# Performance work log

Hardware: AMD Instinct MI355X
Metric: run time of the kernel (lower is better)

The kernel has to match this reference:

```python
import jax, jax.numpy as jnp
import numpy as np

D = 768
H = 12
HD = D // H
NQ = 100
KV = 257
SEQ = NQ + KV
BS = 32


def layer_norm(x, g, b):
    # torch LayerNorm computed in fp32 then cast back (LayerNorm subclass)
    xf = x.astype(jnp.float32)
    m = xf.mean(-1, keepdims=True)
    v = ((xf - m) ** 2).mean(-1, keepdims=True)
    return ((xf - m) / jnp.sqrt(v + 1e-5) * g + b).astype(x.dtype)


def setup_inputs() -> dict:
    key = jax.random.key(0)
    ks = jax.random.split(key, 8)
    s = 0.02
    return {
        "y": jax.random.normal(ks[0], (SEQ, BS, D), jnp.float32),
        "attn_mask": jax.random.bernoulli(ks[1], 0.3, (BS, NQ, KV)),
        "in_proj_w": jax.random.normal(ks[2], (3 * D, D), jnp.float32) * s,
        "in_proj_b": jnp.zeros((3 * D,), jnp.float32),
        "new_q_w": jax.random.normal(ks[3], (D, D), jnp.float32) * s,
        "new_q_b": jnp.zeros((D,), jnp.float32),
        "out_w": jax.random.normal(ks[4], (D, D), jnp.float32) * s,
        "out_b": jnp.zeros((D,), jnp.float32),
        "ln1_g": jnp.ones((D,), jnp.float32),
        "ln1_b": jnp.zeros((D,), jnp.float32),
        "ln2_g": jnp.ones((D,), jnp.float32),
        "ln2_b": jnp.zeros((D,), jnp.float32),
        "fc_w": jax.random.normal(ks[5], (4 * D, D), jnp.float32) * s,
        "fc_b": jnp.zeros((4 * D,), jnp.float32),
        "proj_w": jax.random.normal(ks[6], (D, 4 * D), jnp.float32) * s,
        "proj_b": jnp.zeros((D,), jnp.float32),
    }


def _attention(x, attn_mask, in_proj_w, in_proj_b, new_q_w, new_q_b, out_w, out_b):
    # x: [seq, bs, D] (already ln_1'd); attn_mask: [bs, nq, kv] bool
    seq, bs, d = x.shape
    nq = attn_mask.shape[1]
    scale = 1.0 / np.sqrt(HD)
    # k/v (and the clip queries) come from the detached non-query tokens
    xkv = jax.lax.stop_gradient(x[nq:])  # [kv, bs, D]
    qkv = xkv @ in_proj_w.T + in_proj_b
    q, k, v = jnp.split(qkv, 3, axis=-1)

    def heads(t):  # [S, bs, D] -> [bs, H, S, hd]
        return t.reshape(t.shape[0], bs, H, HD).transpose(1, 2, 0, 3)

    q = heads(q) * scale
    k = heads(k)
    v = heads(v)
    # regular (clip) attention over shared k/v
    clip_attn = jnp.einsum('bhld,bhmd->bhlm', q, k)
    clip_out = jnp.einsum('bhlm,bhmd->bhld', jax.nn.softmax(clip_attn, axis=-1), v)
    # mask-conditioned queries via new_q_proj (NOT detached)
    new_q = heads(x[:nq] @ new_q_w.T + new_q_b) * scale  # [bs, H, nq, hd]
    bias = jnp.where(attn_mask[:, None], -jnp.inf, 0.0).astype(q.dtype)  # [bs,1,nq,kv]
    mask_attn = jnp.einsum('bhqd,bhmd->bhqm', new_q, k) + bias
    mask_out = jnp.einsum('bhqm,bhmd->bhqd', jax.nn.softmax(mask_attn, axis=-1), v)

    def merge(t):  # [bs, H, S, hd] -> [S, bs, D]
        return t.transpose(2, 0, 1, 3).reshape(t.shape[2], bs, d)

    attn_out = jnp.concatenate([merge(mask_out), merge(clip_out)], axis=0)
    return attn_out @ out_w.T + out_b


def reference(y, attn_mask, in_proj_w, in_proj_b, new_q_w, new_q_b, out_w, out_b,
              ln1_g, ln1_b, ln2_g, ln2_b, fc_w, fc_b, proj_w, proj_b):
    x = layer_norm(y, ln1_g, ln1_b)
    y = y + _attention(x, attn_mask, in_proj_w, in_proj_b, new_q_w, new_q_b, out_w, out_b)
    h = layer_norm(y, ln2_g, ln2_b)
    h = h @ fc_w.T + fc_b
    h = h * jax.nn.sigmoid(1.702 * h)  # QuickGELU
    return y + (h @ proj_w.T + proj_b)
```

## Files before the change

### kernel.cpp

```cpp
#include <hip/hip_runtime.h>


typedef short bf16x8 __attribute__((ext_vector_type(8)));
typedef float f32x4 __attribute__((ext_vector_type(4)));
typedef unsigned short u16;
typedef unsigned long long u64;

__device__ __forceinline__ u16 f2b(float f) {
    unsigned u = __builtin_bit_cast(unsigned, f);
    u = (u + 0x7fffu + ((u >> 16) & 1u)) >> 16;
    return (u16)u;
}
__device__ __forceinline__ float b2f(u16 h) {
    unsigned u = ((unsigned)h) << 16;
    return __builtin_bit_cast(float, u);
}
__device__ __forceinline__ unsigned pack2(float a, float b) {
    return (unsigned)f2b(a) | ((unsigned)f2b(b) << 16);
}
__device__ __forceinline__ void g2l16(const void* g, void* l) {
    __builtin_amdgcn_global_load_lds(
        (__attribute__((address_space(1))) void*)g,
        (__attribute__((address_space(3))) void*)l, 16, 0, 0);
}
#define MFMA16(a, b, c) __builtin_amdgcn_mfma_f32_16x16x32_bf16((a), (b), (c), 0, 0, 0)

__global__ __launch_bounds__(256) void cvt5_kernel(
    const float* __restrict__ s0, const float* __restrict__ s1, const float* __restrict__ s2,
    const float* __restrict__ s3, const float* __restrict__ s4, u16* __restrict__ dst)
{
    int i = blockIdx.x * 256 + threadIdx.x;
    int stride = gridDim.x * 256;
    for (; i < 1916928; i += stride) {
        const float* src; int off;
        if (i < 442368)       { src = s0; off = i; }
        else if (i < 589824)  { src = s1; off = i - 442368; }
        else if (i < 737280)  { src = s2; off = i - 589824; }
        else if (i < 1327104) { src = s3; off = i - 737280; }
        else                  { src = s4; off = i - 1327104; }
        float4 v = ((const float4*)src)[off];
        ushort4 o;
        o.x = f2b(v.x); o.y = f2b(v.y); o.z = f2b(v.z); o.w = f2b(v.w);
        ((ushort4*)dst)[i] = o;
    }
}

__global__ __launch_bounds__(256) void mask_pack(const int* __restrict__ m, u64* __restrict__ o) {
    int row = blockIdx.x * 4 + (threadIdx.x >> 6);
    int lane = threadIdx.x & 63;
    if (row >= 3200) return;
    const int* r = m + (size_t)row * 257;
    u64 w0 = __ballot(r[lane] != 0);
    u64 w1 = __ballot(r[64 + lane] != 0);
    u64 w2 = __ballot(r[128 + lane] != 0);
    u64 w3 = __ballot(r[192 + lane] != 0);
    u64 w4 = __ballot(lane == 0 && r[256] != 0);
    if (lane == 0) {
        u64* p = o + (size_t)row * 5;
        p[0] = w0; p[1] = w1; p[2] = w2; p[3] = w3; p[4] = w4;
    }
}

__global__ __launch_bounds__(256) void ln_kernel(
    const float* __restrict__ in, const float* __restrict__ g, const float* __restrict__ be,
    u16* __restrict__ out, int nrows)
{
    int row = blockIdx.x * 4 + (threadIdx.x >> 6);
    int lane = threadIdx.x & 63;
    if (row >= nrows) return;
    const float* p = in + (size_t)row * 768;
    float4 a0 = *(const float4*)(p + lane * 4);
    float4 a1 = *(const float4*)(p + 256 + lane * 4);
    float4 a2 = *(const float4*)(p + 512 + lane * 4);
    float s = a0.x + a0.y + a0.z + a0.w + a1.x + a1.y + a1.z + a1.w + a2.x + a2.y + a2.z + a2.w;
    for (int o = 32; o; o >>= 1) s += __shfl_xor(s, o);
    float mean = s * (1.f / 768.f);
    float vs = 0.f;
#define SQA(t) { float dx; dx = t.x-mean; vs += dx*dx; dx = t.y-mean; vs += dx*dx; dx = t.z-mean; vs += dx*dx; dx = t.w-mean; vs += dx*dx; }
    SQA(a0) SQA(a1) SQA(a2)
#undef SQA
    for (int o = 32; o; o >>= 1) vs += __shfl_xor(vs, o);
    float rstd = rsqrtf(vs * (1.f / 768.f) + 1e-5f);
    u16* orow = out + (size_t)row * 768;
#pragma unroll
    for (int i = 0; i < 3; ++i) {
        int d = i * 256 + lane * 4;
        float4 av = (i == 0) ? a0 : ((i == 1) ? a1 : a2);
        float4 gv = *(const float4*)(g + d);
        float4 bv = *(const float4*)(be + d);
        ushort4 ov;
        ov.x = f2b((av.x - mean) * rstd * gv.x + bv.x);
        ov.y = f2b((av.y - mean) * rstd * gv.y + bv.y);
        ov.z = f2b((av.z - mean) * rstd * gv.z + bv.z);
        ov.w = f2b((av.w - mean) * rstd * gv.w + bv.w);
        *(ushort4*)(orow + d) = ov;
    }
}

template<int ACT, int OUTBF, int RES>
__global__ __launch_bounds__(256) void gemm_bt(
    const u16* __restrict__ A, const u16* __restrict__ B,
    const float* __restrict__ bias, const float* __restrict__ res,
    void* __restrict__ Cp, int M, int N, int K)
{
    __shared__ u16 Al[2][128 * 32];
    __shared__ u16 Bl[2][128 * 32];
    const int t = threadIdx.x;
    const int lane = t & 63, w = t >> 6;
    const int wr = w >> 1, wc = w & 1;
    const int fr = lane & 15, fg = lane >> 4;

    const int raw = blockIdx.x + gridDim.x * blockIdx.y;
    const int rows_per = gridDim.x >> 3;
    const int gy = gridDim.y;
    const int xcd = raw & 7, idx = raw >> 3;
    const int nt = idx % gy;
    const int mt = xcd * rows_per + idx / gy;
    const int m0 = mt * 128, n0 = nt * 128;
    if (m0 >= M) return;

    const int srow = lane >> 2;
    const int scol = (lane & 3) * 8;
    int ar0 = m0 + w * 32 + srow;      int ar1 = ar0 + 16;
    ar0 = ar0 < M ? ar0 : M - 1;       ar1 = ar1 < M ? ar1 : M - 1;
    int br0 = n0 + w * 32 + srow;      int br1 = br0 + 16;
    br0 = br0 < N ? br0 : N - 1;       br1 = br1 < N ? br1 : N - 1;
    const u16* a0p = A + (size_t)ar0 * K + scol;
    const u16* a1p = A + (size_t)ar1 * K + scol;
    const u16* b0p = B + (size_t)br0 * K + scol;
    const u16* b1p = B + (size_t)br1 * K + scol;
    const int lo0 = (w * 2 + 0) * 512, lo1 = (w * 2 + 1) * 512;

    const int nk = K >> 5;
    g2l16(a0p, &Al[0][lo0]);
    g2l16(a1p, &Al[0][lo1]);
    g2l16(b0p, &Bl[0][lo0]);
    g2l16(b1p, &Bl[0][lo1]);
    __syncthreads();

    f32x4 acc[4][4] = {};
#pragma unroll 2
    for (int ki = 0; ki < nk; ++ki) {
        const int cur = ki & 1;
        if (ki + 1 < nk) {
            const int k0 = (ki + 1) << 5;
            const int nxt = cur ^ 1;
            g2l16(a0p + k0, &Al[nxt][lo0]);
            g2l16(a1p + k0, &Al[nxt][lo1]);
            g2l16(b0p + k0, &Bl[nxt][lo0]);
            g2l16(b1p + k0, &Bl[nxt][lo1]);
        }
        bf16x8 af[4], bfr[4];
#pragma unroll
        for (int m = 0; m < 4; ++m) af[m] = *(const bf16x8*)&Al[cur][(wr * 64 + m * 16 + fr) * 32 + fg * 8];
#pragma unroll
        for (int n = 0; n < 4; ++n) bfr[n] = *(const bf16x8*)&Bl[cur][(wc * 64 + n * 16 + fr) * 32 + fg * 8];
#pragma unroll
        for (int m = 0; m < 4; ++m)
#pragma unroll
            for (int n = 0; n < 4; ++n)
                acc[m][n] = MFMA16(af[m], bfr[n], acc[m][n]);
        __syncthreads();
    }
#pragma unroll
    for (int m = 0; m < 4; ++m) {
#pragma unroll
        for (int n = 0; n < 4; ++n) {
            int col = n0 + wc * 64 + n * 16 + fr;
            float bv = bias[col];
#pragma unroll
            for (int r = 0; r < 4; ++r) {
                int row = m0 + wr * 64 + m * 16 + fg * 4 + r;
                if (row < M) {
                    float v = acc[m][n][r] + bv;
                    if (RES) v += res[(size_t)row * N + col];
                    if (ACT) v = v / (1.f + __expf(-1.702f * v));
                    if (OUTBF) ((u16*)Cp)[(size_t)row * N + col] = f2b(v);
                    else       ((float*)Cp)[(size_t)row * N + col] = v;
                }
            }
        }
    }
}

template<int ACT, int OUTBF, int RES>
__global__ __launch_bounds__(256) void gemm_bt64(
    const u16* __restrict__ A, const u16* __restrict__ B,
    const float* __restrict__ bias, const float* __restrict__ res,
    void* __restrict__ Cp, int M, int N, int K)
{
    __shared__ u16 Al[2][128 * 64];
    __shared__ u16 Bl[2][128 * 64];
    const int t = threadIdx.x;
    const int lane = t & 63, w = t >> 6;
    const int wr = w >> 1, wc = w & 1;
    const int fr = lane & 15, fg = lane >> 4;

    const int raw = blockIdx.x + gridDim.x * blockIdx.y;
    const int rows_per = gridDim.x >> 3;
    const int gy = gridDim.y;
    const int xcd = raw & 7, idx = raw >> 3;
    const int nt = idx % gy;
    const int mt = xcd * rows_per + idx / gy;
    const int m0 = mt * 128, n0 = nt * 128;
    if (m0 >= M) return;

    const int srow = lane >> 3;
    const int scol = ((lane & 7) ^ srow) * 8;
    const u16* ap[4];
    const u16* bp[4];
#pragma unroll
    for (int j = 0; j < 4; ++j) {
        int ar = m0 + w * 32 + j * 8 + srow;  ar = ar < M ? ar : M - 1;
        ap[j] = A + (size_t)ar * K + scol;
        int br = n0 + w * 32 + j * 8 + srow;  br = br < N ? br : N - 1;
        bp[j] = B + (size_t)br * K + scol;
    }
    const int lbase = w * 2048;

    const int nk = K >> 6;
    {
#pragma unroll
        for (int j = 0; j < 4; ++j) {
            g2l16(ap[j], &Al[0][lbase + j * 512]);
            g2l16(bp[j], &Bl[0][lbase + j * 512]);
        }
    }
    __syncthreads();

    f32x4 acc[4][4] = {};
    const int swz = fr & 7;
#pragma unroll 2
    for (int ki = 0; ki < nk; ++ki) {
        const int cur = ki & 1;
        if (ki + 1 < nk) {
            const int k0 = (ki + 1) << 6;
            const int nxt = cur ^ 1;
#pragma unroll
            for (int j = 0; j < 4; ++j) {
                g2l16(ap[j] + k0, &Al[nxt][lbase + j * 512]);
                g2l16(bp[j] + k0, &Bl[nxt][lbase + j * 512]);
            }
        }
        const char* ab = (const char*)&Al[cur][0];
        const char* bb = (const char*)&Bl[cur][0];
#pragma unroll
        for (int s = 0; s < 2; ++s) {
            bf16x8 af[4], bfr[4];
            const int slot = ((fg + 4 * s) ^ swz) << 4;
#pragma unroll
            for (int m = 0; m < 4; ++m)
                af[m] = *(const bf16x8*)(ab + (wr * 64 + m * 16 + fr) * 128 + slot);
#pragma unroll
            for (int n = 0; n < 4; ++n)
                bfr[n] = *(const bf16x8*)(bb + (wc * 64 + n * 16 + fr) * 128 + slot);
#pragma unroll
            for (int m = 0; m < 4; ++m)
#pragma unroll
                for (int n = 0; n < 4; ++n)
                    acc[m][n] = MFMA16(af[m], bfr[n], acc[m][n]);
        }
        __syncthreads();
    }
#pragma unroll
    for (int m = 0; m < 4; ++m) {
#pragma unroll
        for (int n = 0; n < 4; ++n) {
            int col = n0 + wc * 64 + n * 16 + fr;
            float bv = bias[col];
#pragma unroll
            for (int r = 0; r < 4; ++r) {
                int row = m0 + wr * 64 + m * 16 + fg * 4 + r;
                if (row < M) {
                    float v = acc[m][n][r] + bv;
                    if (RES) v += res[(size_t)row * N + col];
                    if (ACT) v = v / (1.f + __expf(-1.702f * v));
                    if (OUTBF) ((u16*)Cp)[(size_t)row * N + col] = f2b(v);
                    else       ((float*)Cp)[(size_t)row * N + col] = v;
                }
            }
        }
    }
}

__global__ __launch_bounds__(256, 2) void attn_kernel(
    const u16* __restrict__ qkv,
    const u16* __restrict__ nq,
    const u64* __restrict__ mpk,
    u16* __restrict__ out)
{
    __shared__ u16 Kl[272 * 64];
    __shared__ u16 Vt[64 * 296];
    const int raw = blockIdx.x;
    const int bid = (raw & 7) * 48 + (raw >> 3);
    const int b = bid / 12, h = bid % 12;
    const int t = threadIdx.x, lane = t & 63, wv = t >> 6;
    const int fr = lane & 15, fg = lane >> 4;

    for (int i = t; i < 2048; i += 256) {
        int d = i >> 5, c = 257 + (i & 31);
        if (c < 288) Vt[d * 296 + c] = 0;
    }
    {
        const int r8 = t >> 3, c8 = (t & 7) * 8;
        const u16* kb = qkv + 768 + h * 64 + c8;
        const u16* vb = qkv + 1536 + h * 64 + c8;
#pragma unroll 1
        for (int p = 0; p < 9; ++p) {
            int m = r8 + p * 32;
            if (m <= 256) {
                size_t go = (size_t)(m * 32 + b) * 2304;
                bf16x8 kv = *(const bf16x8*)(kb + go);
                int byte = m * 128 + c8 * 2;
                *(bf16x8*)((char*)Kl + (byte ^ ((m & 7) << 4))) = kv;
                bf16x8 vv = *(const bf16x8*)(vb + go);
#pragma unroll
                for (int j = 0; j < 8; ++j)
                    Vt[(c8 + j) * 296 + m] = (u16)vv[j];
            }
        }
    }
    __syncthreads();

    const int swzK = (fr & 7) << 4;
    const char* KlB = (const char*)Kl;
    const char* VtB = (const char*)Vt;
    const int psrc0 = fr + 32 * (fg & 1);
    const int psrc1 = psrc0 + 16;
    const bool phi = fg >= 2;

    auto fetch = [&](int ti, bf16x8& q0v, bf16x8& q1v, u64* mw, bool& im) {
        int q = ti * 16 + fr;
        int qc = q < 357 ? q : 356;
        im = qc < 100;
        const u16* qp = im ? (nq + (size_t)(qc * 32 + b) * 768 + h * 64)
                           : (qkv + (size_t)((qc - 100) * 32 + b) * 2304 + h * 64);
        q0v = *(const bf16x8*)(qp + fg * 8);
        q1v = *(const bf16x8*)(qp + 32 + fg * 8);
        if (im) {
            const u64* mp = mpk + (size_t)(b * 100 + qc) * 5;
            mw[0] = mp[0]; mw[1] = mp[1]; mw[2] = mp[2]; mw[3] = mp[3]; mw[4] = mp[4];
        } else {
            mw[0] = mw[1] = mw[2] = mw[3] = mw[4] = 0;
        }
    };

    bf16x8 qf0, qf1, qn0, qn1;
    u64 mwc[5], mwn[5];
    bool imc, imn;
    fetch(wv, qf0, qf1, mwc, imc);

#pragma unroll 1
    for (int ti = wv; ti < 23; ti += 4) {
        f32x4 sc[17];
#pragma unroll
        for (int kt = 0; kt < 17; ++kt) {
            int rb = (kt * 16 + fr) * 128;
            bf16x8 ka0 = *(const bf16x8*)(KlB + ((rb + fg * 16) ^ swzK));
            bf16x8 ka1 = *(const bf16x8*)(KlB + ((rb + 64 + fg * 16) ^ swzK));
            f32x4 a = {0.f, 0.f, 0.f, 0.f};
            a = MFMA16(ka0, qf0, a);
            a = MFMA16(ka1, qf1, a);
            sc[kt] = a;
        }
        if (ti + 4 < 23) fetch(ti + 4, qn0, qn1, mwn, imn);
        float tm[17];
#pragma unroll
        for (int kt = 0; kt < 17; ++kt) {
            u64 mw = (kt >> 2) == 0 ? mwc[0] : (kt >> 2) == 1 ? mwc[1] : (kt >> 2) == 2 ? mwc[2]
                   : (kt >> 2) == 3 ? mwc[3] : mwc[4];
            float s0, s1, s2, s3;
            {
                int key = kt * 16 + fg * 4;
                bool b0 = (key > 256) || (imc && ((mw >> (key & 63)) & 1ull));
                bool b1 = (key + 1 > 256) || (imc && ((mw >> ((key + 1) & 63)) & 1ull));
                bool b2 = (key + 2 > 256) || (imc && ((mw >> ((key + 2) & 63)) & 1ull));
                bool b3 = (key + 3 > 256) || (imc && ((mw >> ((key + 3) & 63)) & 1ull));
                s0 = b0 ? -INFINITY : sc[kt][0];
                s1 = b1 ? -INFINITY : sc[kt][1];
                s2 = b2 ? -INFINITY : sc[kt][2];
                s3 = b3 ? -INFINITY : sc[kt][3];
            }
            sc[kt][0] = s0; sc[kt][1] = s1; sc[kt][2] = s2; sc[kt][3] = s3;
            tm[kt] = fmaxf(fmaxf(s0, s1), fmaxf(s2, s3));
        }
        float m8_0 = fmaxf(tm[0], tm[8]),  m8_1 = fmaxf(tm[1], tm[9]);
        float m8_2 = fmaxf(tm[2], tm[10]), m8_3 = fmaxf(tm[3], tm[11]);
        float m8_4 = fmaxf(tm[4], tm[12]), m8_5 = fmaxf(tm[5], tm[13]);
        float m8_6 = fmaxf(tm[6], tm[14]), m8_7 = fmaxf(tm[7], tm[15]);
        float m4_0 = fmaxf(m8_0, m8_4), m4_1 = fmaxf(m8_1, m8_5);
        float m4_2 = fmaxf(m8_2, m8_6), m4_3 = fmaxf(m8_3, m8_7);
        float mx = fmaxf(fmaxf(fmaxf(m4_0, m4_1), fmaxf(m4_2, m4_3)), tm[16]);
        mx = fmaxf(mx, __shfl_xor(mx, 16));
        mx = fmaxf(mx, __shfl_xor(mx, 32));
        float l = 0.f;
        unsigned pk[17][2];
#pragma unroll
        for (int kt = 0; kt < 17; ++kt) {
            float p0 = __expf((sc[kt][0] - mx) * 0.125f);
            float p1 = __expf((sc[kt][1] - mx) * 0.125f);
            float p2 = __expf((sc[kt][2] - mx) * 0.125f);
            float p3 = __expf((sc[kt][3] - mx) * 0.125f);
            l += (p0 + p1) + (p2 + p3);
            pk[kt][0] = pack2(p0, p1);
            pk[kt][1] = pack2(p2, p3);
        }
        l += __shfl_xor(l, 16);
        l += __shfl_xor(l, 32);
        f32x4 oc[4] = {};
#pragma unroll
        for (int c = 0; c < 9; ++c) {
            unsigned p00 = pk[2 * c][0], p01 = pk[2 * c][1];
            unsigned p10 = (c < 8) ? pk[2 * c + 1][0] : 0u;
            unsigned p11 = (c < 8) ? pk[2 * c + 1][1] : 0u;
            unsigned a00 = __shfl(p00, psrc0), a01 = __shfl(p01, psrc0);
            unsigned a10 = __shfl(p10, psrc0), a11 = __shfl(p11, psrc0);
            unsigned b00 = __shfl(p00, psrc1), b01 = __shfl(p01, psrc1);
            unsigned b10 = __shfl(p10, psrc1), b11 = __shfl(p11, psrc1);
            uint4 pw;
            pw.x = phi ? a10 : a00;  pw.y = phi ? a11 : a01;
            pw.z = phi ? b10 : b00;  pw.w = phi ? b11 : b01;
            bf16x8 pf = __builtin_bit_cast(bf16x8, pw);
#pragma unroll
            for (int dt = 0; dt < 4; ++dt) {
                bf16x8 vf = *(const bf16x8*)(VtB + (dt * 16 + fr) * 592 + c * 64 + fg * 16);
                oc[dt] = MFMA16(vf, pf, oc[dt]);
            }
        }
        int q = ti * 16 + fr;
        if (q < 357) {
            float rl = 1.f / l;
            u16* op = out + (size_t)(q * 32 + b) * 768 + h * 64 + fg * 4;
#pragma unroll
            for (int dt = 0; dt < 4; ++dt) {
                ushort4 ov;
                ov.x = f2b(oc[dt][0] * rl); ov.y = f2b(oc[dt][1] * rl);
                ov.z = f2b(oc[dt][2] * rl); ov.w = f2b(oc[dt][3] * rl);
                *(ushort4*)(op + dt * 16) = ov;
            }
        }
        if (ti + 4 < 23) {
            qf0 = qn0; qf1 = qn1; imc = imn;
            mwc[0] = mwn[0]; mwc[1] = mwn[1]; mwc[2] = mwn[2]; mwc[3] = mwn[3]; mwc[4] = mwn[4];
        }
    }
}

extern "C" void kernel_launch(void* const* d_in, const int* in_sizes, int n_in,
                              void* d_out, int out_size, void* d_ws, size_t ws_size,
                              hipStream_t stream)
{
    const float* y   = (const float*)d_in[0];
    const int*   msk = (const int*)  d_in[1];
    const float* ipw = (const float*)d_in[2];
    const float* ipb = (const float*)d_in[3];
    const float* nqw = (const float*)d_in[4];
    const float* nqb = (const float*)d_in[5];
    const float* ow  = (const float*)d_in[6];
    const float* ob  = (const float*)d_in[7];
    const float* l1g = (const float*)d_in[8];
    const float* l1b = (const float*)d_in[9];
    const float* l2g = (const float*)d_in[10];
    const float* l2b = (const float*)d_in[11];
    const float* fcw = (const float*)d_in[12];
    const float* fcb = (const float*)d_in[13];
    const float* pjw = (const float*)d_in[14];
    const float* pjb = (const float*)d_in[15];

    char* ws = (char*)d_ws;
    u16* x_b   = (u16*)(ws + 0);
    u16* qkv_b = (u16*)(ws + 17547264);
    u16* nq_b  = (u16*)(ws + 55443456);
    u16* ao_b  = (u16*)(ws + 60358656);
    u16* h1_b  = (u16*)(ws + 0);
    u16* h_b   = (u16*)(ws + 77905920);
    u64* mpk_b = (u64*)(ws + 77905920);
    u16* w_ip  = (u16*)(ws + 95453184);
    float* out = (float*)d_out;

    cvt5_kernel<<<2048, 256, 0, stream>>>(ipw, nqw, ow, fcw, pjw, w_ip);
    mask_pack<<<800, 256, 0, stream>>>(msk, mpk_b);

    u16* w_nq  = w_ip + 1769472;
    u16* w_out = w_nq + 589824;
    u16* w_fc  = w_out + 589824;
    u16* w_pj  = w_fc + 2359296;

    ln_kernel<<<2856, 256, 0, stream>>>(y, l1g, l1b, x_b, 11424);
    gemm_bt<0, 1, 0><<<dim3(72, 18), 256, 0, stream>>>(x_b + (size_t)3200 * 768, w_ip, ipb, nullptr, qkv_b, 8224, 2304, 768);
    gemm_bt<0, 1, 0><<<dim3(32, 6), 256, 0, stream>>>(x_b, w_nq, nqb, nullptr, nq_b, 3200, 768, 768);
    attn_kernel<<<384, 256, 0, stream>>>(qkv_b, nq_b, mpk_b, ao_b);
    gemm_bt<0, 0, 1><<<dim3(96, 6), 256, 0, stream>>>(ao_b, w_out, ob, y, out, 11424, 768, 768);
    ln_kernel<<<2856, 256, 0, stream>>>(out, l2g, l2b, h_b, 11424);
    gemm_bt64<1, 1, 0><<<dim3(96, 24), 256, 0, stream>>>(h_b, w_fc, fcb, nullptr, h1_b, 11424, 3072, 768);
    gemm_bt64<0, 0, 1><<<dim3(96, 6), 256, 0, stream>>>(h1_b, w_pj, pjb, out, out, 11424, 768, 3072);
}
```

Before: 489.3 us.

## Use per-wave private LDS staging to drop block barriers in MLP GEMMs

Replaces the shared, block-synchronised double-buffered GEMM for the MLP fc and proj layers with a variant where each wave stages its own A and B slices into a private LDS region. Completion is tracked with explicit vmcnt waits instead of __syncthreads. K per stage drops from 64 to 32 and the XOR swizzle is removed. This aims to remove barrier stalls between waves, at the cost of redundant global loads (each row slice is fetched by two waves), more loop iterations, and possible LDS bank conflicts.

```diff
diff --git a/kernel.cpp b/kernel.cpp
--- a/kernel.cpp
+++ b/kernel.cpp
@@ -24,6 +24,10 @@
         (__attribute__((address_space(3))) void*)l, 16, 0, 0);
 }
 #define MFMA16(a, b, c) __builtin_amdgcn_mfma_f32_16x16x32_bf16((a), (b), (c), 0, 0, 0)
+#define VMW8() do { asm volatile("s_waitcnt vmcnt(8)" ::: "memory"); \
+                    __builtin_amdgcn_sched_barrier(0); } while (0)
+#define VMW0() do { asm volatile("s_waitcnt vmcnt(0)" ::: "memory"); \
+                    __builtin_amdgcn_sched_barrier(0); } while (0)
 
 __global__ __launch_bounds__(256) void cvt5_kernel(
     const float* __restrict__ s0, const float* __restrict__ s1, const float* __restrict__ s2,
@@ -184,13 +188,12 @@
 }
 
 template<int ACT, int OUTBF, int RES>
-__global__ __launch_bounds__(256) void gemm_bt64(
+__global__ __launch_bounds__(256) void gemm_nb(
     const u16* __restrict__ A, const u16* __restrict__ B,
     const float* __restrict__ bias, const float* __restrict__ res,
     void* __restrict__ Cp, int M, int N, int K)
 {
-    __shared__ u16 Al[2][128 * 64];
-    __shared__ u16 Bl[2][128 * 64];
+    __shared__ u16 L[4 * 2 * 2 * 2048];
     const int t = threadIdx.x;
     const int lane = t & 63, w = t >> 6;
     const int wr = w >> 1, wc = w & 1;
@@ -205,62 +208,51 @@
     const int m0 = mt * 128, n0 = nt * 128;
     if (m0 >= M) return;
 
-    const int srow = lane >> 3;
-    const int scol = ((lane & 7) ^ srow) * 8;
-    const u16* ap[4];
-    const u16* bp[4];
+    const int srow = lane >> 2;
+    const int scol = (lane & 3) * 8;
+    const u16* apg[4];
+    const u16* bpg[4];
 #pragma unroll
     for (int j = 0; j < 4; ++j) {
-        int ar = m0 + w * 32 + j * 8 + srow;  ar = ar < M ? ar : M - 1;
-        ap[j] = A + (size_t)ar * K + scol;
-        int br = n0 + w * 32 + j * 8 + srow;  br = br < N ? br : N - 1;
-        bp[j] = B + (size_t)br * K + scol;
-    }
-    const int lbase = w * 2048;
-
-    const int nk = K >> 6;
-    {
-#pragma unroll
-        for (int j = 0; j < 4; ++j) {
-            g2l16(ap[j], &Al[0][lbase + j * 512]);
-            g2l16(bp[j], &Bl[0][lbase + j * 512]);
-        }
-    }
-    __syncthreads();
-
+        int ar = m0 + wr * 64 + j * 16 + srow;  ar = ar < M ? ar : M - 1;
+        apg[j] = A + (size_t)ar * K + scol;
+        int br = n0 + wc * 64 + j * 16 + srow;  br = br < N ? br : N - 1;
+        bpg[j] = B + (size_t)br * K + scol;
+    }
+    u16* const wbase = &L[w * 8192];
+    auto stage = [&](int ki, int bsel) {
+        const int k0 = ki << 5;
+        u16* la = wbase + bsel * 4096;
+#pragma unroll
+        for (int j = 0; j < 4; ++j) g2l16(apg[j] + k0, la + j * 512);
+#pragma unroll
+        for (int j = 0; j < 4; ++j) g2l16(bpg[j] + k0, la + 2048 + j * 512);
+    };
+
+    const int nk = K >> 5;
+    stage(0, 0);
     f32x4 acc[4][4] = {};
-    const int swz = fr & 7;
 #pragma unroll 2
     for (int ki = 0; ki < nk; ++ki) {
         const int cur = ki & 1;
         if (ki + 1 < nk) {
-            const int k0 = (ki + 1) << 6;
-            const int nxt = cur ^ 1;
-#pragma unroll
-            for (int j = 0; j < 4; ++j) {
-                g2l16(ap[j] + k0, &Al[nxt][lbase + j * 512]);
-                g2l16(bp[j] + k0, &Bl[nxt][lbase + j * 512]);
-            }
-        }
-        const char* ab = (const char*)&Al[cur][0];
-        const char* bb = (const char*)&Bl[cur][0];
-#pragma unroll
-        for (int s = 0; s < 2; ++s) {
-            bf16x8 af[4], bfr[4];
-            const int slot = ((fg + 4 * s) ^ swz) << 4;
-#pragma unroll
-            for (int m = 0; m < 4; ++m)
-                af[m] = *(const bf16x8*)(ab + (wr * 64 + m * 16 + fr) * 128 + slot);
+            stage(ki + 1, cur ^ 1);
+            VMW8();
+        } else {
+            VMW0();
+        }
+        const u16* la = wbase + cur * 4096;
+        const u16* lb = la + 2048;
+        bf16x8 af[4], bfr[4];
+#pragma unroll
+        for (int m = 0; m < 4; ++m) af[m] = *(const bf16x8*)&la[(m * 16 + fr) * 32 + fg * 8];
+#pragma unroll
+        for (int n = 0; n < 4; ++n) bfr[n] = *(const bf16x8*)&lb[(n * 16 + fr) * 32 + fg * 8];
+#pragma unroll
+        for (int m = 0; m < 4; ++m)
 #pragma unroll
             for (int n = 0; n < 4; ++n)
-                bfr[n] = *(const bf16x8*)(bb + (wc * 64 + n * 16 + fr) * 128 + slot);
-#pragma unroll
-            for (int m = 0; m < 4; ++m)
-#pragma unroll
-                for (int n = 0; n < 4; ++n)
-                    acc[m][n] = MFMA16(af[m], bfr[n], acc[m][n]);
-        }
-        __syncthreads();
+                acc[m][n] = MFMA16(af[m], bfr[n], acc[m][n]);
     }
 #pragma unroll
     for (int m = 0; m < 4; ++m) {
@@ -492,6 +484,6 @@
     attn_kernel<<<384, 256, 0, stream>>>(qkv_b, nq_b, mpk_b, ao_b);
     gemm_bt<0, 0, 1><<<dim3(96, 6), 256, 0, stream>>>(ao_b, w_out, ob, y, out, 11424, 768, 768);
     ln_kernel<<<2856, 256, 0, stream>>>(out, l2g, l2b, h_b, 11424);
-    gemm_bt64<1, 1, 0><<<dim3(96, 24), 256, 0, stream>>>(h_b, w_fc, fcb, nullptr, h1_b, 11424, 3072, 768);
-    gemm_bt64<0, 0, 1><<<dim3(96, 6), 256, 0, stream>>>(h1_b, w_pj, pjb, out, out, 11424, 768, 3072);
-}
+    gemm_nb<1, 1, 0><<<dim3(96, 24), 256, 0, stream>>>(h_b, w_fc, fcb, nullptr, h1_b, 11424, 3072, 768);
+    gemm_nb<0, 0, 1><<<dim3(96, 6), 256, 0, stream>>>(h1_b, w_pj, pjb, out, out, 11424, 768, 3072);
+}
```

Result: slower. 534.1 us (+9.2%).
